# Kernel optimization log

Hardware: AMD Instinct MI355X
Metric: run time of the kernel (lower is better)

## Reference

```python
import jax, jax.numpy as jnp
import numpy as np

N_NODES = 100000
N_EDGES = 1600000
IN_CH = 165


def setup_inputs() -> dict:
    key = jax.random.key(0)
    ks = jax.random.split(key, 6)
    x = jax.random.normal(ks[0], (N_NODES, IN_CH), dtype=jnp.float32)
    edge_index = jax.random.randint(ks[1], (2, N_EDGES), 0, N_NODES, dtype=jnp.int32)
    # Glorot-ish init for weights
    W1 = jax.random.normal(ks[2], (IN_CH, 128), dtype=jnp.float32) * (1.0 / np.sqrt(IN_CH))
    b1 = jnp.zeros((128,), dtype=jnp.float32)
    W2 = jax.random.normal(ks[3], (128, 64), dtype=jnp.float32) * (1.0 / np.sqrt(128))
    b2 = jnp.zeros((64,), dtype=jnp.float32)
    Wo = jax.random.normal(ks[4], (64, 2), dtype=jnp.float32) * (1.0 / np.sqrt(64))
    bo = jnp.zeros((2,), dtype=jnp.float32)
    return {"x": x, "edge_index": edge_index, "W1": W1, "b1": b1,
            "W2": W2, "b2": b2, "Wo": Wo, "bo": bo}


def _gcn_norm(edge_index, n_nodes, dtype):
    """Add self-loops and compute symmetric normalization deg^-1/2 * deg^-1/2 (PyG gcn_norm)."""
    loops = jnp.arange(n_nodes, dtype=edge_index.dtype)
    ei = jnp.concatenate([edge_index, jnp.stack([loops, loops])], axis=1)
    row, col = ei[0], ei[1]
    deg = jax.ops.segment_sum(jnp.ones(ei.shape[1], dtype), col, num_segments=n_nodes)
    deg_inv_sqrt = jnp.where(deg > 0, jax.lax.rsqrt(deg), 0.0)
    norm = deg_inv_sqrt[row] * deg_inv_sqrt[col]  # [E+N]
    return row, col, norm


def _gcn_conv(h, row, col, norm, W, b, n_nodes):
    # transform first (F_in -> F_out), then gather-scale-scatter aggregate
    m = h @ W                                   # [N, F_out]
    msg = m[row] * norm[:, None]                # [E+N, F_out]
    agg = jax.ops.segment_sum(msg, col, num_segments=n_nodes)
    return agg + b


def reference(x, edge_index, W1, b1, W2, b2, Wo, bo):
    n_nodes = x.shape[0]
    row, col, norm = _gcn_norm(edge_index, n_nodes, x.dtype)
    h = jax.nn.relu(_gcn_conv(x, row, col, norm, W1, b1, n_nodes))
    h = jax.nn.relu(_gcn_conv(h, row, col, norm, W2, b2, n_nodes))
    return h @ Wo + bo  # [N, 2] logits
```

## Files before the change

kernel.cpp:

```cpp
#include <hip/hip_runtime.h>

#define N_NODES 100000
#define N_EDGES 1600000
#define IN_CH   165
#define BSHIFT 7
#define NBUCK  ((N_NODES + 127) / 128)
#define BCAP   3072
#define PA_BLOCKS 256
#define WSPLIT_BLOCKS 128
#define G1_BLOCKS ((N_NODES + 63) / 64)

typedef unsigned short ushort_t;
typedef _Float16 f16;
typedef _Float16 f16x8 __attribute__((ext_vector_type(8)));
typedef _Float16 hfrag8 __attribute__((ext_vector_type(8)));
typedef short bfrag8 __attribute__((ext_vector_type(8)));
typedef float f32x4 __attribute__((ext_vector_type(4)));

__device__ __forceinline__ ushort_t f2bf(float f) {
    unsigned u = __float_as_uint(f);
    unsigned r = (u + 0x7fffu + ((u >> 16) & 1u)) >> 16;
    return (ushort_t)r;
}
__device__ __forceinline__ float bf2f(ushort_t h) {
    return __uint_as_float(((unsigned)h) << 16);
}

__device__ __forceinline__ void fmix_lo(float& a, unsigned pair, float s) {
    asm("v_fma_mix_f32 %0, %1, %2, %0 op_sel_hi:[1,0,0]" : "+v"(a) : "v"(pair), "v"(s));
}
__device__ __forceinline__ void fmix_hi(float& a, unsigned pair, float s) {
    asm("v_fma_mix_f32 %0, %1, %2, %0 op_sel:[1,0,0] op_sel_hi:[1,0,0]" : "+v"(a) : "v"(pair), "v"(s));
}
__device__ __forceinline__ void fmix_acc8(float* acc, uint4 v, float s) {
    fmix_lo(acc[0], v.x, s); fmix_hi(acc[1], v.x, s);
    fmix_lo(acc[2], v.y, s); fmix_hi(acc[3], v.y, s);
    fmix_lo(acc[4], v.z, s); fmix_hi(acc[5], v.z, s);
    fmix_lo(acc[6], v.w, s); fmix_hi(acc[7], v.w, s);
}

__global__ void bucketA_kernel(const int* __restrict__ row, const int* __restrict__ col,
                               int* __restrict__ bfill, unsigned* __restrict__ tmp,
                               const float* __restrict__ W1, const float* __restrict__ W2,
                               ushort_t* __restrict__ wt1h, ushort_t* __restrict__ wt1l,
                               ushort_t* __restrict__ wt2h, ushort_t* __restrict__ wt2l) {
    __shared__ int lcnt[NBUCK];
    __shared__ int lcur[NBUCK];
    int t = threadIdx.x;
    if (blockIdx.x >= PA_BLOCKS) {
        int i = (blockIdx.x - PA_BLOCKS) * 256 + t;
        if (i < 128 * 192) {
            int ch = i / 192, k = i - ch * 192;
            float v = (k < IN_CH) ? W1[(size_t)k * 128 + ch] : 0.f;
            ushort_t h = f2bf(v);
            wt1h[i] = h;
            wt1l[i] = f2bf(v - bf2f(h));
        } else if (i < 128 * 192 + 64 * 128) {
            int j = i - 128 * 192;
            int ch = j / 128, k = j - ch * 128;
            float v = W2[(size_t)k * 64 + ch];
            f16 h = (f16)v;
            f16 l = (f16)(v - (float)h);
            wt2h[j] = *(ushort_t*)&h;
            wt2l[j] = *(ushort_t*)&l;
        }
        return;
    }
    int e0 = (int)((long)blockIdx.x * N_EDGES / PA_BLOCKS);
    int e1 = (int)((long)(blockIdx.x + 1) * N_EDGES / PA_BLOCKS);
    for (int i = t; i < NBUCK; i += 256) lcnt[i] = 0;
    __syncthreads();
    for (int e = e0 + t; e < e1; e += 256)
        atomicAdd(&lcnt[col[e] >> BSHIFT], 1);
    __syncthreads();
    for (int b = t; b < NBUCK; b += 256) {
        int c = lcnt[b];
        lcur[b] = (c > 0) ? (b * BCAP + atomicAdd(&bfill[b], c)) : 0;
    }
    __syncthreads();
    for (int e = e0 + t; e < e1; e += 256) {
        int cc = col[e];
        int b = cc >> BSHIFT;
        int p = atomicAdd(&lcur[b], 1);
        tmp[p] = ((unsigned)(cc & 127) << 17) | (unsigned)row[e];
    }
}

__launch_bounds__(256)
__global__ void b2g1_kernel(const unsigned* __restrict__ tmp, const int* __restrict__ bfill,
                            float* __restrict__ dis, int* __restrict__ off,
                            unsigned* __restrict__ srt,
                            const float* __restrict__ X,
                            const ushort_t* __restrict__ wth, const ushort_t* __restrict__ wtl,
                            f16* __restrict__ M, int n_nodes) {
    __shared__ char smem[20480];
    int t = threadIdx.x;
    int lane = t & 63, wid = t >> 6;
    if (blockIdx.x < NBUCK) {
        int* lcnt = (int*)smem;
        int* wred = (int*)(smem + 512);
        int* sh   = (int*)(smem + 1024);
        int* lcur = (int*)(smem + 1536);
        int b = blockIdx.x;
        if (t < 128) lcnt[t] = 0;
        __syncthreads();
        int total = min(bfill[b], BCAP);
        const unsigned* reg = tmp + (size_t)b * BCAP;
        for (int i = t; i < total; i += 256)
            atomicAdd(&lcnt[(reg[i] >> 17) & 127], 1);
        int s = 0;
        for (int j = t; j < b; j += 256) s += bfill[j];
        #pragma unroll
        for (int o = 32; o > 0; o >>= 1) s += __shfl_xor(s, o);
        if (lane == 0) wred[wid] = s;
        __syncthreads();
        int base = wred[0] + wred[1] + wred[2] + wred[3];
        int myc = 0;
        if (t < 128) {
            myc = lcnt[t];
            int n = (b << BSHIFT) + t;
            if (n < N_NODES) dis[n] = rsqrtf((float)(myc + 1));
            sh[t] = myc;
        }
        __syncthreads();
        for (int o = 1; o < 128; o <<= 1) {
            int x = (t < 128 && t >= o) ? sh[t - o] : 0;
            __syncthreads();
            if (t < 128) sh[t] += x;
            __syncthreads();
        }
        if (t < 128) {
            int excl = sh[t] - myc;
            int n = (b << BSHIFT) + t;
            if (n < N_NODES) off[n] = base + excl;
            lcur[t] = excl;
        }
        if (b == 0 && t == 0) off[N_NODES] = N_EDGES;
        __syncthreads();
        for (int i = t; i < total; i += 256) {
            unsigned e = reg[i];
            int c = (e >> 17) & 127;
            int p = atomicAdd(&lcur[c], 1);
            srt[base + p] = e & 0x1FFFFu;
        }
        return;
    }
    constexpr int XP = 40;
    ushort_t (*wsh)[XP] = (ushort_t(*)[XP])smem;
    ushort_t (*wsl)[XP] = (ushort_t(*)[XP])(smem + 10240);

    int bid = blockIdx.x - NBUCK;
    long node0 = (long)bid * 64;
    int r = (int)node0 + wid * 16 + (lane & 15);
    int rr = min(r, n_nodes - 1);
    int q = lane >> 4;
    const float* xrow = X + (size_t)rr * IN_CH;

    f32x4 acc[8];
    #pragma unroll
    for (int ct = 0; ct < 8; ++ct) acc[ct] = (f32x4){0.f, 0.f, 0.f, 0.f};

    bfrag8 wfh[2], wfl[2];
    float a[8];

    auto loadW = [&](int c) {
        int k0 = c * 32;
        #pragma unroll
        for (int i = 0; i < 2; ++i) {
            int idx = t + i * 256;
            int ch = idx >> 2, qq = idx & 3;
            wfh[i] = *(const bfrag8*)&wth[(size_t)ch * 192 + k0 + qq * 8];
            wfl[i] = *(const bfrag8*)&wtl[(size_t)ch * 192 + k0 + qq * 8];
        }
    };
    auto storeW = [&]() {
        #pragma unroll
        for (int i = 0; i < 2; ++i) {
            int idx = t + i * 256;
            int ch = idx >> 2, qq = idx & 3;
            *(bfrag8*)&wsh[ch][qq * 8] = wfh[i];
            *(bfrag8*)&wsl[ch][qq * 8] = wfl[i];
        }
    };
    auto loadX = [&](int c) {
        int k = c * 32 + q * 8;
        if (c < 5) {
            #pragma unroll
            for (int i = 0; i < 8; ++i) a[i] = xrow[k + i];
        } else {
            #pragma unroll
            for (int i = 0; i < 8; ++i) a[i] = 0.f;
            if (q == 0) {
                a[0] = xrow[160]; a[1] = xrow[161]; a[2] = xrow[162];
                a[3] = xrow[163]; a[4] = xrow[164];
            }
        }
    };

    loadW(0);
    loadX(0);
    #pragma unroll 1
    for (int c = 0; c < 6; ++c) {
        storeW();
        __syncthreads();
        if (c + 1 < 6) loadW(c + 1);
        bfrag8 ah, al;
        #pragma unroll
        for (int i = 0; i < 8; ++i) {
            ushort_t h = (ushort_t)(__float_as_uint(a[i]) >> 16);
            ah[i] = (short)h;
            al[i] = (short)f2bf(a[i] - bf2f(h));
        }
        if (c + 1 < 6) loadX(c + 1);
        #pragma unroll
        for (int ct = 0; ct < 8; ++ct) {
            bfrag8 bh = *(const bfrag8*)&wsh[ct * 16 + (lane & 15)][q * 8];
            bfrag8 bl = *(const bfrag8*)&wsl[ct * 16 + (lane & 15)][q * 8];
            acc[ct] = __builtin_amdgcn_mfma_f32_16x16x32_bf16(ah, bh, acc[ct], 0, 0, 0);
            acc[ct] = __builtin_amdgcn_mfma_f32_16x16x32_bf16(ah, bl, acc[ct], 0, 0, 0);
            acc[ct] = __builtin_amdgcn_mfma_f32_16x16x32_bf16(al, bh, acc[ct], 0, 0, 0);
        }
        __syncthreads();
    }

    int nl = wid * 16 + (lane >> 4) * 4;
    #pragma unroll
    for (int ct = 0; ct < 8; ++ct) {
        int ch = ct * 16 + (lane & 15);
        #pragma unroll
        for (int j = 0; j < 4; ++j) {
            long node = node0 + nl + j;
            if (node < n_nodes)
                M[node * 128 + ch] = (f16)acc[ct][j];
        }
    }
}

__launch_bounds__(256)
__global__ void gemm2_kernel(const f16* __restrict__ H,
                             const ushort_t* __restrict__ wth, const ushort_t* __restrict__ wtl,
                             f16* __restrict__ M, int n_nodes) {
    constexpr int XP = 40;
    __shared__ ushort_t wsh[64][XP];
    __shared__ ushort_t wsl[64][XP];
    int t = threadIdx.x;
    int l = t & 63, wid = t >> 6;
    long node0 = (long)blockIdx.x * 64;
    int r = (int)node0 + wid * 16 + (l & 15);
    int rr = min(r, n_nodes - 1);
    int q = l >> 4;
    const f16* hrow = H + (size_t)rr * 128;

    f32x4 acc[4];
    #pragma unroll
    for (int ct = 0; ct < 4; ++ct) acc[ct] = (f32x4){0.f, 0.f, 0.f, 0.f};

    bfrag8 wfh, wfl;
    auto loadW = [&](int c) {
        int ch = t >> 2, qq = t & 3;
        wfh = *(const bfrag8*)&wth[(size_t)ch * 128 + c * 32 + qq * 8];
        wfl = *(const bfrag8*)&wtl[(size_t)ch * 128 + c * 32 + qq * 8];
    };
    auto storeW = [&]() {
        int ch = t >> 2, qq = t & 3;
        *(bfrag8*)&wsh[ch][qq * 8] = wfh;
        *(bfrag8*)&wsl[ch][qq * 8] = wfl;
    };

    loadW(0);
    hfrag8 a = *(const hfrag8*)&hrow[q * 8];
    #pragma unroll 1
    for (int c = 0; c < 4; ++c) {
        storeW();
        __syncthreads();
        if (c + 1 < 4) loadW(c + 1);
        hfrag8 acur = a;
        if (c + 1 < 4) a = *(const hfrag8*)&hrow[(c + 1) * 32 + q * 8];
        #pragma unroll
        for (int ct = 0; ct < 4; ++ct) {
            hfrag8 bh = *(const hfrag8*)&wsh[ct * 16 + (l & 15)][q * 8];
            hfrag8 bl = *(const hfrag8*)&wsl[ct * 16 + (l & 15)][q * 8];
            acc[ct] = __builtin_amdgcn_mfma_f32_16x16x32_f16(acur, bh, acc[ct], 0, 0, 0);
            acc[ct] = __builtin_amdgcn_mfma_f32_16x16x32_f16(acur, bl, acc[ct], 0, 0, 0);
        }
        __syncthreads();
    }

    int nl = wid * 16 + (l >> 4) * 4;
    #pragma unroll
    for (int ct = 0; ct < 4; ++ct) {
        int ch = ct * 16 + (l & 15);
        #pragma unroll
        for (int j = 0; j < 4; ++j) {
            long node = node0 + nl + j;
            if (node < n_nodes)
                M[node * 64 + ch] = (f16)acc[ct][j];
        }
    }
}

__global__ void agg1_kernel(const f16* __restrict__ ms, const unsigned* __restrict__ srt,
                            const int* __restrict__ off, const float* __restrict__ dis,
                            const float* __restrict__ b1, f16* __restrict__ h1) {
    int wave = threadIdx.x >> 6;
    int lane = threadIdx.x & 63;
    int n = blockIdx.x * 4 + wave;
    if (n >= N_NODES) return;
    int g = lane >> 4, p = lane & 15;
    const char* msb = (const char*)ms;
    unsigned pb = (unsigned)p * 16;
    int s0 = off[n], s1 = off[n + 1];
    float dn = rsqrtf((float)(s1 - s0) + 1.f);
    float acc[8] = {0.f, 0.f, 0.f, 0.f, 0.f, 0.f, 0.f, 0.f};
    if (g == 0) {
        uint4 v = *(const uint4*)(msb + (unsigned)n * 256 + pb);
        fmix_acc8(acc, v, dn);
    }
    unsigned sv = (s0 + lane < s1) ? srt[s0 + lane] : 0;
    for (int base = s0; base < s1; base += 64) {
        int nb2 = base + 64;
        unsigned svn = (nb2 + lane < s1) ? srt[nb2 + lane] : 0;
        int cnt_ = min(64, s1 - base);
        int j = 0;
        for (; j + 15 < cnt_; j += 16) {
            unsigned e0 = (unsigned)__shfl((int)sv, j + g);
            unsigned e1 = (unsigned)__shfl((int)sv, j + 4 + g);
            unsigned e2 = (unsigned)__shfl((int)sv, j + 8 + g);
            unsigned e3 = (unsigned)__shfl((int)sv, j + 12 + g);
            uint4 v0 = *(const uint4*)(msb + e0 * 256 + pb);
            uint4 v1 = *(const uint4*)(msb + e1 * 256 + pb);
            uint4 v2 = *(const uint4*)(msb + e2 * 256 + pb);
            uint4 v3 = *(const uint4*)(msb + e3 * 256 + pb);
            float d0 = dis[e0];
            float d1 = dis[e1];
            float d2 = dis[e2];
            float d3 = dis[e3];
            fmix_acc8(acc, v0, d0);
            fmix_acc8(acc, v1, d1);
            fmix_acc8(acc, v2, d2);
            fmix_acc8(acc, v3, d3);
        }
        for (; j < cnt_; j += 4) {
            unsigned e = (unsigned)__shfl((int)sv, j + g);
            float ws = (j + g < cnt_) ? dis[e] : 0.f;
            uint4 v = *(const uint4*)(msb + e * 256 + pb);
            fmix_acc8(acc, v, ws);
        }
        sv = svn;
    }
    #pragma unroll
    for (int i = 0; i < 8; ++i) {
        acc[i] += __shfl_xor(acc[i], 16);
        acc[i] += __shfl_xor(acc[i], 32);
    }
    if (lane < 16) {
        float4 ba = ((const float4*)b1)[lane * 2];
        float4 bb = ((const float4*)b1)[lane * 2 + 1];
        float bv[8] = {ba.x, ba.y, ba.z, ba.w, bb.x, bb.y, bb.z, bb.w};
        f16x8 r;
        #pragma unroll
        for (int i = 0; i < 8; ++i)
            r[i] = (f16)fmaxf(acc[i] * dn + bv[i], 0.f);
        *(f16x8*)(h1 + (size_t)n * 128 + lane * 8) = r;
    }
}

__global__ void agg2_kernel(const f16* __restrict__ ms, const unsigned* __restrict__ srt,
                            const int* __restrict__ off, const float* __restrict__ dis,
                            const float* __restrict__ b2, const float* __restrict__ Wo,
                            const float* __restrict__ bo, float* __restrict__ out) {
    int wave = threadIdx.x >> 6;
    int lane = threadIdx.x & 63;
    int n = blockIdx.x * 4 + wave;
    if (n >= N_NODES) return;
    int g = lane >> 3, p = lane & 7;
    const char* msb = (const char*)ms;
    unsigned pb = (unsigned)p * 16;
    int s0 = off[n], s1 = off[n + 1];
    float dn = rsqrtf((float)(s1 - s0) + 1.f);
    float acc[8] = {0.f, 0.f, 0.f, 0.f, 0.f, 0.f, 0.f, 0.f};
    if (g == 0) {
        uint4 v = *(const uint4*)(msb + (unsigned)n * 128 + pb);
        fmix_acc8(acc, v, dn);
    }
    unsigned sv = (s0 + lane < s1) ? srt[s0 + lane] : 0;
    for (int base = s0; base < s1; base += 64) {
        int nb2 = base + 64;
        unsigned svn = (nb2 + lane < s1) ? srt[nb2 + lane] : 0;
        int cnt_ = min(64, s1 - base);
        int j = 0;
        for (; j + 15 < cnt_; j += 16) {
            unsigned e0 = (unsigned)__shfl((int)sv, j + g);
            unsigned e1 = (unsigned)__shfl((int)sv, j + 8 + g);
            uint4 v0 = *(const uint4*)(msb + e0 * 128 + pb);
            uint4 v1 = *(const uint4*)(msb + e1 * 128 + pb);
            float d0 = dis[e0];
            float d1 = dis[e1];
            fmix_acc8(acc, v0, d0);
            fmix_acc8(acc, v1, d1);
        }
        for (; j < cnt_; j += 8) {
            unsigned e = (unsigned)__shfl((int)sv, j + g);
            float ws = (j + g < cnt_) ? dis[e] : 0.f;
            uint4 v = *(const uint4*)(msb + e * 128 + pb);
            fmix_acc8(acc, v, ws);
        }
        sv = svn;
    }
    #pragma unroll
    for (int i = 0; i < 8; ++i) {
        acc[i] += __shfl_xor(acc[i], 8);
        acc[i] += __shfl_xor(acc[i], 16);
        acc[i] += __shfl_xor(acc[i], 32);
    }
    float p0 = 0.f, p1 = 0.f;
    #pragma unroll
    for (int i = 0; i < 8; ++i) {
        int ch = p * 8 + i;
        float hc = fmaxf(acc[i] * dn + b2[ch], 0.f);
        p0 = fmaf(hc, Wo[ch * 2], p0);
        p1 = fmaf(hc, Wo[ch * 2 + 1], p1);
    }
    p0 += __shfl_xor(p0, 1); p1 += __shfl_xor(p1, 1);
    p0 += __shfl_xor(p0, 2); p1 += __shfl_xor(p1, 2);
    p0 += __shfl_xor(p0, 4); p1 += __shfl_xor(p1, 4);
    if (lane == 0) {
        out[(size_t)n * 2]     = p0 + bo[0];
        out[(size_t)n * 2 + 1] = p1 + bo[1];
    }
}

extern "C" void kernel_launch(void* const* d_in, const int* in_sizes, int n_in,
                              void* d_out, int out_size, void* d_ws, size_t ws_size,
                              hipStream_t stream) {
    const float* x  = (const float*)d_in[0];
    const int*   ei = (const int*)d_in[1];
    const int*   row = ei;
    const int*   col = ei + N_EDGES;
    const float* W1 = (const float*)d_in[2];
    const float* b1 = (const float*)d_in[3];
    const float* W2 = (const float*)d_in[4];
    const float* b2 = (const float*)d_in[5];
    const float* Wo = (const float*)d_in[6];
    const float* bo = (const float*)d_in[7];
    float* out = (float*)d_out;

    char* base = (char*)d_ws;
    auto alloc = [&](size_t bytes) {
        char* p = base;
        base += (bytes + 255) & ~(size_t)255;
        return p;
    };
    float*    dis  = (float*)alloc((size_t)N_NODES * 4);
    int*      off  = (int*)alloc((size_t)(N_NODES + 1) * 4);
    int*      bfill= (int*)alloc((size_t)NBUCK * 4);
    unsigned* tmp  = (unsigned*)alloc((size_t)NBUCK * BCAP * 4 + 4096);
    unsigned* srt  = (unsigned*)alloc((size_t)N_EDGES * 4);
    f16*      m    = (f16*)alloc((size_t)N_NODES * 128 * 2);
    f16*      h1   = (f16*)alloc((size_t)N_NODES * 128 * 2);
    ushort_t* wt1h = (ushort_t*)alloc((size_t)128 * 192 * 2);
    ushort_t* wt1l = (ushort_t*)alloc((size_t)128 * 192 * 2);
    ushort_t* wt2h = (ushort_t*)alloc((size_t)64 * 128 * 2);
    ushort_t* wt2l = (ushort_t*)alloc((size_t)64 * 128 * 2);

    hipMemsetAsync(bfill, 0, (size_t)NBUCK * 4, stream);

    bucketA_kernel<<<PA_BLOCKS + WSPLIT_BLOCKS, 256, 0, stream>>>(
        row, col, bfill, tmp, W1, W2, wt1h, wt1l, wt2h, wt2l);

    b2g1_kernel<<<NBUCK + G1_BLOCKS, 256, 0, stream>>>(
        tmp, bfill, dis, off, srt, x, wt1h, wt1l, m, N_NODES);

    agg1_kernel<<<(N_NODES + 3) / 4, 256, 0, stream>>>(m, srt, off, dis, b1, h1);

    gemm2_kernel<<<G1_BLOCKS, 256, 0, stream>>>(h1, wt2h, wt2l, m, N_NODES);
    agg2_kernel<<<(N_NODES + 3) / 4, 256, 0, stream>>>(m, srt, off, dis, b2, Wo, bo, out);
}
```

Before: 209.5 us.

## Fuse layer-2 GEMM into layer-1 aggregation kernel via LDS and MFMA

The layer-1 aggregation kernel now keeps each block's four aggregated, ReLU'd node rows in shared memory (padded to 16 rows with zeros) and immediately multiplies them by W2 with f16 MFMA (hi/lo split), writing the 64-channel layer-2 messages directly. This removes the h1 intermediate buffer round trip and a separate GEMM launch. The cost is that 12 of 16 MFMA rows are wasted padding, every block re-reads W2 fragments from global memory, and a block barrier is added after the gather.

```diff
diff --git a/kernel.cpp b/kernel.cpp
--- a/kernel.cpp
+++ b/kernel.cpp
@@ -236,76 +236,21 @@
     }
 }
 
-__launch_bounds__(256)
-__global__ void gemm2_kernel(const f16* __restrict__ H,
-                             const ushort_t* __restrict__ wth, const ushort_t* __restrict__ wtl,
-                             f16* __restrict__ M, int n_nodes) {
-    constexpr int XP = 40;
-    __shared__ ushort_t wsh[64][XP];
-    __shared__ ushort_t wsl[64][XP];
+__global__ void agg1g2_kernel(const f16* __restrict__ ms, const unsigned* __restrict__ srt,
+                              const int* __restrict__ off, const float* __restrict__ dis,
+                              const float* __restrict__ b1,
+                              const ushort_t* __restrict__ wt2h, const ushort_t* __restrict__ wt2l,
+                              f16* __restrict__ m2) {
+    __shared__ f16 lds_h[16][136];
     int t = threadIdx.x;
-    int l = t & 63, wid = t >> 6;
-    long node0 = (long)blockIdx.x * 64;
-    int r = (int)node0 + wid * 16 + (l & 15);
-    int rr = min(r, n_nodes - 1);
-    int q = l >> 4;
-    const f16* hrow = H + (size_t)rr * 128;
-
-    f32x4 acc[4];
-    #pragma unroll
-    for (int ct = 0; ct < 4; ++ct) acc[ct] = (f32x4){0.f, 0.f, 0.f, 0.f};
-
-    bfrag8 wfh, wfl;
-    auto loadW = [&](int c) {
-        int ch = t >> 2, qq = t & 3;
-        wfh = *(const bfrag8*)&wth[(size_t)ch * 128 + c * 32 + qq * 8];
-        wfl = *(const bfrag8*)&wtl[(size_t)ch * 128 + c * 32 + qq * 8];
-    };
-    auto storeW = [&]() {
-        int ch = t >> 2, qq = t & 3;
-        *(bfrag8*)&wsh[ch][qq * 8] = wfh;
-        *(bfrag8*)&wsl[ch][qq * 8] = wfl;
-    };
-
-    loadW(0);
-    hfrag8 a = *(const hfrag8*)&hrow[q * 8];
-    #pragma unroll 1
-    for (int c = 0; c < 4; ++c) {
-        storeW();
-        __syncthreads();
-        if (c + 1 < 4) loadW(c + 1);
-        hfrag8 acur = a;
-        if (c + 1 < 4) a = *(const hfrag8*)&hrow[(c + 1) * 32 + q * 8];
-        #pragma unroll
-        for (int ct = 0; ct < 4; ++ct) {
-            hfrag8 bh = *(const hfrag8*)&wsh[ct * 16 + (l & 15)][q * 8];
-            hfrag8 bl = *(const hfrag8*)&wsl[ct * 16 + (l & 15)][q * 8];
-            acc[ct] = __builtin_amdgcn_mfma_f32_16x16x32_f16(acur, bh, acc[ct], 0, 0, 0);
-            acc[ct] = __builtin_amdgcn_mfma_f32_16x16x32_f16(acur, bl, acc[ct], 0, 0, 0);
-        }
-        __syncthreads();
-    }
-
-    int nl = wid * 16 + (l >> 4) * 4;
-    #pragma unroll
-    for (int ct = 0; ct < 4; ++ct) {
-        int ch = ct * 16 + (l & 15);
-        #pragma unroll
-        for (int j = 0; j < 4; ++j) {
-            long node = node0 + nl + j;
-            if (node < n_nodes)
-                M[node * 64 + ch] = (f16)acc[ct][j];
-        }
-    }
-}
-
-__global__ void agg1_kernel(const f16* __restrict__ ms, const unsigned* __restrict__ srt,
-                            const int* __restrict__ off, const float* __restrict__ dis,
-                            const float* __restrict__ b1, f16* __restrict__ h1) {
-    int wave = threadIdx.x >> 6;
-    int lane = threadIdx.x & 63;
-    int n = blockIdx.x * 4 + wave;
-    if (n >= N_NODES) return;
+    int wid = t >> 6;
+    int lane = t & 63;
+    f16x8 zz = {};
+    for (int i = t; i < 192; i += 256) {
+        int rw = 4 + (i >> 4), cl = (i & 15) * 8;
+        *(f16x8*)&lds_h[rw][cl] = zz;
+    }
+    int n = blockIdx.x * 4 + wid;
     int g = lane >> 4, p = lane & 15;
     const char* msb = (const char*)ms;
     unsigned pb = (unsigned)p * 16;
@@ -361,7 +306,28 @@
         #pragma unroll
         for (int i = 0; i < 8; ++i)
             r[i] = (f16)fmaxf(acc[i] * dn + bv[i], 0.f);
-        *(f16x8*)(h1 + (size_t)n * 128 + lane * 8) = r;
+        *(f16x8*)&lds_h[wid][lane * 8] = r;
+    }
+    __syncthreads();
+    {
+        int q = lane >> 4, cl = lane & 15;
+        const ushort_t* bhp = wt2h + ((size_t)(wid * 16 + cl)) * 128 + q * 8;
+        const ushort_t* blp = wt2l + ((size_t)(wid * 16 + cl)) * 128 + q * 8;
+        f32x4 acc2 = (f32x4){0.f, 0.f, 0.f, 0.f};
+        #pragma unroll
+        for (int c = 0; c < 4; ++c) {
+            hfrag8 a2 = *(const hfrag8*)&lds_h[cl][c * 32 + q * 8];
+            hfrag8 bh = *(const hfrag8*)&bhp[c * 32];
+            hfrag8 bl = *(const hfrag8*)&blp[c * 32];
+            acc2 = __builtin_amdgcn_mfma_f32_16x16x32_f16(a2, bh, acc2, 0, 0, 0);
+            acc2 = __builtin_amdgcn_mfma_f32_16x16x32_f16(a2, bl, acc2, 0, 0, 0);
+        }
+        if (q == 0) {
+            long nb = (long)blockIdx.x * 4;
+            #pragma unroll
+            for (int j = 0; j < 4; ++j)
+                m2[(nb + j) * 64 + wid * 16 + cl] = (f16)acc2[j];
+        }
     }
 }
 
@@ -457,7 +423,7 @@
     unsigned* tmp  = (unsigned*)alloc((size_t)NBUCK * BCAP * 4 + 4096);
     unsigned* srt  = (unsigned*)alloc((size_t)N_EDGES * 4);
     f16*      m    = (f16*)alloc((size_t)N_NODES * 128 * 2);
-    f16*      h1   = (f16*)alloc((size_t)N_NODES * 128 * 2);
+    f16*      m2   = (f16*)alloc((size_t)N_NODES * 64 * 2);
     ushort_t* wt1h = (ushort_t*)alloc((size_t)128 * 192 * 2);
     ushort_t* wt1l = (ushort_t*)alloc((size_t)128 * 192 * 2);
     ushort_t* wt2h = (ushort_t*)alloc((size_t)64 * 128 * 2);
@@ -471,8 +437,7 @@
     b2g1_kernel<<<NBUCK + G1_BLOCKS, 256, 0, stream>>>(
         tmp, bfill, dis, off, srt, x, wt1h, wt1l, m, N_NODES);
 
-    agg1_kernel<<<(N_NODES + 3) / 4, 256, 0, stream>>>(m, srt, off, dis, b1, h1);
-
-    gemm2_kernel<<<G1_BLOCKS, 256, 0, stream>>>(h1, wt2h, wt2l, m, N_NODES);
-    agg2_kernel<<<(N_NODES + 3) / 4, 256, 0, stream>>>(m, srt, off, dis, b2, Wo, bo, out);
-}
+    agg1g2_kernel<<<N_NODES / 4, 256, 0, stream>>>(m, srt, off, dis, b1, wt2h, wt2l, m2);
+
+    agg2_kernel<<<(N_NODES + 3) / 4, 256, 0, stream>>>(m2, srt, off, dis, b2, Wo, bo, out);
+}
```

Measured after the change: 261.5 us. 1.25x slower.

## Regroup preprocessing kernels to overlap edge bucketing with first GEMM

Applied to the files above, without the earlier changes.

Weight splitting and bfill zeroing move into a small standalone kernel, which replaces the memset. Edge bucketing pass A now shares a launch with the layer-1 GEMM, and bucket pass B becomes its own kernel. The aim is to overlap the scatter-heavy, atomic-bound bucketing with the compute-bound GEMM, rather than overlapping pass B with the GEMM. Kernel count stays the same (the memset is dropped, a kernel is added). The standalone pass B kernel may run with less overlap than before.

```diff
diff --git a/kernel.cpp b/kernel.cpp
--- a/kernel.cpp
+++ b/kernel.cpp
@@ -39,109 +39,58 @@
     fmix_lo(acc[6], v.w, s); fmix_hi(acc[7], v.w, s);
 }
 
-__global__ void bucketA_kernel(const int* __restrict__ row, const int* __restrict__ col,
-                               int* __restrict__ bfill, unsigned* __restrict__ tmp,
-                               const float* __restrict__ W1, const float* __restrict__ W2,
-                               ushort_t* __restrict__ wt1h, ushort_t* __restrict__ wt1l,
-                               ushort_t* __restrict__ wt2h, ushort_t* __restrict__ wt2l) {
-    __shared__ int lcnt[NBUCK];
-    __shared__ int lcur[NBUCK];
-    int t = threadIdx.x;
-    if (blockIdx.x >= PA_BLOCKS) {
-        int i = (blockIdx.x - PA_BLOCKS) * 256 + t;
-        if (i < 128 * 192) {
-            int ch = i / 192, k = i - ch * 192;
-            float v = (k < IN_CH) ? W1[(size_t)k * 128 + ch] : 0.f;
-            ushort_t h = f2bf(v);
-            wt1h[i] = h;
-            wt1l[i] = f2bf(v - bf2f(h));
-        } else if (i < 128 * 192 + 64 * 128) {
-            int j = i - 128 * 192;
-            int ch = j / 128, k = j - ch * 128;
-            float v = W2[(size_t)k * 64 + ch];
-            f16 h = (f16)v;
-            f16 l = (f16)(v - (float)h);
-            wt2h[j] = *(ushort_t*)&h;
-            wt2l[j] = *(ushort_t*)&l;
-        }
-        return;
-    }
-    int e0 = (int)((long)blockIdx.x * N_EDGES / PA_BLOCKS);
-    int e1 = (int)((long)(blockIdx.x + 1) * N_EDGES / PA_BLOCKS);
-    for (int i = t; i < NBUCK; i += 256) lcnt[i] = 0;
-    __syncthreads();
-    for (int e = e0 + t; e < e1; e += 256)
-        atomicAdd(&lcnt[col[e] >> BSHIFT], 1);
-    __syncthreads();
-    for (int b = t; b < NBUCK; b += 256) {
-        int c = lcnt[b];
-        lcur[b] = (c > 0) ? (b * BCAP + atomicAdd(&bfill[b], c)) : 0;
-    }
-    __syncthreads();
-    for (int e = e0 + t; e < e1; e += 256) {
-        int cc = col[e];
-        int b = cc >> BSHIFT;
-        int p = atomicAdd(&lcur[b], 1);
-        tmp[p] = ((unsigned)(cc & 127) << 17) | (unsigned)row[e];
+__global__ void wsplit_kernel(const float* __restrict__ W1, const float* __restrict__ W2,
+                              ushort_t* __restrict__ wt1h, ushort_t* __restrict__ wt1l,
+                              ushort_t* __restrict__ wt2h, ushort_t* __restrict__ wt2l,
+                              int* __restrict__ bfill) {
+    int i = blockIdx.x * 256 + threadIdx.x;
+    if (i < NBUCK) bfill[i] = 0;
+    if (i < 128 * 192) {
+        int ch = i / 192, k = i - ch * 192;
+        float v = (k < IN_CH) ? W1[(size_t)k * 128 + ch] : 0.f;
+        ushort_t h = f2bf(v);
+        wt1h[i] = h;
+        wt1l[i] = f2bf(v - bf2f(h));
+    } else if (i < 128 * 192 + 64 * 128) {
+        int j = i - 128 * 192;
+        int ch = j / 128, k = j - ch * 128;
+        float v = W2[(size_t)k * 64 + ch];
+        f16 h = (f16)v;
+        f16 l = (f16)(v - (float)h);
+        wt2h[j] = *(ushort_t*)&h;
+        wt2l[j] = *(ushort_t*)&l;
     }
 }
 
 __launch_bounds__(256)
-__global__ void b2g1_kernel(const unsigned* __restrict__ tmp, const int* __restrict__ bfill,
-                            float* __restrict__ dis, int* __restrict__ off,
-                            unsigned* __restrict__ srt,
-                            const float* __restrict__ X,
-                            const ushort_t* __restrict__ wth, const ushort_t* __restrict__ wtl,
-                            f16* __restrict__ M, int n_nodes) {
+__global__ void bucketAg1_kernel(const int* __restrict__ row, const int* __restrict__ col,
+                                 int* __restrict__ bfill, unsigned* __restrict__ tmp,
+                                 const float* __restrict__ X,
+                                 const ushort_t* __restrict__ wth, const ushort_t* __restrict__ wtl,
+                                 f16* __restrict__ M, int n_nodes) {
     __shared__ char smem[20480];
     int t = threadIdx.x;
     int lane = t & 63, wid = t >> 6;
-    if (blockIdx.x < NBUCK) {
+    if (blockIdx.x < PA_BLOCKS) {
         int* lcnt = (int*)smem;
-        int* wred = (int*)(smem + 512);
-        int* sh   = (int*)(smem + 1024);
-        int* lcur = (int*)(smem + 1536);
-        int b = blockIdx.x;
-        if (t < 128) lcnt[t] = 0;
-        __syncthreads();
-        int total = min(bfill[b], BCAP);
-        const unsigned* reg = tmp + (size_t)b * BCAP;
-        for (int i = t; i < total; i += 256)
-            atomicAdd(&lcnt[(reg[i] >> 17) & 127], 1);
-        int s = 0;
-        for (int j = t; j < b; j += 256) s += bfill[j];
-        #pragma unroll
-        for (int o = 32; o > 0; o >>= 1) s += __shfl_xor(s, o);
-        if (lane == 0) wred[wid] = s;
-        __syncthreads();
-        int base = wred[0] + wred[1] + wred[2] + wred[3];
-        int myc = 0;
-        if (t < 128) {
-            myc = lcnt[t];
-            int n = (b << BSHIFT) + t;
-            if (n < N_NODES) dis[n] = rsqrtf((float)(myc + 1));
-            sh[t] = myc;
-        }
-        __syncthreads();
-        for (int o = 1; o < 128; o <<= 1) {
-            int x = (t < 128 && t >= o) ? sh[t - o] : 0;
-            __syncthreads();
-            if (t < 128) sh[t] += x;
-            __syncthreads();
-        }
-        if (t < 128) {
-            int excl = sh[t] - myc;
-            int n = (b << BSHIFT) + t;
-            if (n < N_NODES) off[n] = base + excl;
-            lcur[t] = excl;
-        }
-        if (b == 0 && t == 0) off[N_NODES] = N_EDGES;
-        __syncthreads();
-        for (int i = t; i < total; i += 256) {
-            unsigned e = reg[i];
-            int c = (e >> 17) & 127;
-            int p = atomicAdd(&lcur[c], 1);
-            srt[base + p] = e & 0x1FFFFu;
+        int* lcur = ((int*)smem) + NBUCK;
+        int e0 = (int)((long)blockIdx.x * N_EDGES / PA_BLOCKS);
+        int e1 = (int)((long)(blockIdx.x + 1) * N_EDGES / PA_BLOCKS);
+        for (int i = t; i < NBUCK; i += 256) lcnt[i] = 0;
+        __syncthreads();
+        for (int e = e0 + t; e < e1; e += 256)
+            atomicAdd(&lcnt[col[e] >> BSHIFT], 1);
+        __syncthreads();
+        for (int b = t; b < NBUCK; b += 256) {
+            int c = lcnt[b];
+            lcur[b] = (c > 0) ? (b * BCAP + atomicAdd(&bfill[b], c)) : 0;
+        }
+        __syncthreads();
+        for (int e = e0 + t; e < e1; e += 256) {
+            int cc = col[e];
+            int b = cc >> BSHIFT;
+            int p = atomicAdd(&lcur[b], 1);
+            tmp[p] = ((unsigned)(cc & 127) << 17) | (unsigned)row[e];
         }
         return;
     }
@@ -149,7 +98,7 @@
     ushort_t (*wsh)[XP] = (ushort_t(*)[XP])smem;
     ushort_t (*wsl)[XP] = (ushort_t(*)[XP])(smem + 10240);
 
-    int bid = blockIdx.x - NBUCK;
+    int bid = blockIdx.x - PA_BLOCKS;
     long node0 = (long)bid * 64;
     int r = (int)node0 + wid * 16 + (lane & 15);
     int rr = min(r, n_nodes - 1);
@@ -233,6 +182,59 @@
             if (node < n_nodes)
                 M[node * 128 + ch] = (f16)acc[ct][j];
         }
+    }
+}
+
+__global__ void bucketB_kernel(const unsigned* __restrict__ tmp, const int* __restrict__ bfill,
+                               float* __restrict__ dis, int* __restrict__ off,
+                               unsigned* __restrict__ srt) {
+    __shared__ int lcnt[128];
+    __shared__ int wred[4];
+    __shared__ int sh[128];
+    __shared__ int lcur[128];
+    int t = threadIdx.x;
+    int lane = t & 63, wid = t >> 6;
+    int b = blockIdx.x;
+    if (t < 128) lcnt[t] = 0;
+    __syncthreads();
+    int total = min(bfill[b], BCAP);
+    const unsigned* reg = tmp + (size_t)b * BCAP;
+    for (int i = t; i < total; i += 256)
+        atomicAdd(&lcnt[(reg[i] >> 17) & 127], 1);
+    int s = 0;
+    for (int j = t; j < b; j += 256) s += bfill[j];
+    #pragma unroll
+    for (int o = 32; o > 0; o >>= 1) s += __shfl_xor(s, o);
+    if (lane == 0) wred[wid] = s;
+    __syncthreads();
+    int base = wred[0] + wred[1] + wred[2] + wred[3];
+    int myc = 0;
+    if (t < 128) {
+        myc = lcnt[t];
+        int n = (b << BSHIFT) + t;
+        if (n < N_NODES) dis[n] = rsqrtf((float)(myc + 1));
+        sh[t] = myc;
+    }
+    __syncthreads();
+    for (int o = 1; o < 128; o <<= 1) {
+        int x = (t < 128 && t >= o) ? sh[t - o] : 0;
+        __syncthreads();
+        if (t < 128) sh[t] += x;
+        __syncthreads();
+    }
+    if (t < 128) {
+        int excl = sh[t] - myc;
+        int n = (b << BSHIFT) + t;
+        if (n < N_NODES) off[n] = base + excl;
+        lcur[t] = excl;
+    }
+    if (b == 0 && t == 0) off[N_NODES] = N_EDGES;
+    __syncthreads();
+    for (int i = t; i < total; i += 256) {
+        unsigned e = reg[i];
+        int c = (e >> 17) & 127;
+        int p = atomicAdd(&lcur[c], 1);
+        srt[base + p] = e & 0x1FFFFu;
     }
 }
 
@@ -463,13 +465,12 @@
     ushort_t* wt2h = (ushort_t*)alloc((size_t)64 * 128 * 2);
     ushort_t* wt2l = (ushort_t*)alloc((size_t)64 * 128 * 2);
 
-    hipMemsetAsync(bfill, 0, (size_t)NBUCK * 4, stream);
-
-    bucketA_kernel<<<PA_BLOCKS + WSPLIT_BLOCKS, 256, 0, stream>>>(
-        row, col, bfill, tmp, W1, W2, wt1h, wt1l, wt2h, wt2l);
-
-    b2g1_kernel<<<NBUCK + G1_BLOCKS, 256, 0, stream>>>(
-        tmp, bfill, dis, off, srt, x, wt1h, wt1l, m, N_NODES);
+    wsplit_kernel<<<WSPLIT_BLOCKS, 256, 0, stream>>>(W1, W2, wt1h, wt1l, wt2h, wt2l, bfill);
+
+    bucketAg1_kernel<<<PA_BLOCKS + G1_BLOCKS, 256, 0, stream>>>(
+        row, col, bfill, tmp, x, wt1h, wt1l, m, N_NODES);
+
+    bucketB_kernel<<<NBUCK, 256, 0, stream>>>(tmp, bfill, dis, off, srt);
 
     agg1_kernel<<<(N_NODES + 3) / 4, 256, 0, stream>>>(m, srt, off, dis, b1, h1);
 
```

Measured after the change: 195.5 us. 6.7% less time.
